# Kernel tuning notes

Measured on AMD Instinct MI355X. Metric: run time of the kernel, lower is better.

The kernel has to match this reference:

```python
import jax, jax.numpy as jnp
import numpy as np

MARGIN = 0.1
LAMBDA_EFFECT = 0.5

B, T_V, K, T_S = 32, 8192, 64, 128


def setup_inputs() -> dict:
    key = jax.random.key(0)
    k1, k2, k3, k4, k5 = jax.random.split(key, 5)
    pred_orig = jax.random.normal(k1, (B, T_V), dtype=jnp.float32)
    pred_intervened = jax.random.normal(k2, (K, B, T_V), dtype=jnp.float32)
    intervened_indices = jax.random.randint(k3, (K,), 0, T_S, dtype=jnp.int32)
    # GT alignment mask: sparse-ish binary alignment between frames and sentences
    gt_mask = jax.random.bernoulli(k4, 0.2, (B, T_V, T_S)).astype(jnp.int32)
    # prefix-valid video mask: valid length per batch in [T_V//2, T_V]
    lengths = jax.random.randint(k5, (B,), T_V // 2, T_V + 1, dtype=jnp.int32)
    mask_video = (jnp.arange(T_V, dtype=jnp.int32)[None, :] < lengths[:, None]).astype(jnp.int32)
    return {
        "pred_orig": pred_orig,
        "pred_intervened": pred_intervened,
        "intervened_indices": intervened_indices,
        "gt_mask": gt_mask,
        "mask_video": mask_video,
    }


def reference(pred_orig, pred_intervened, intervened_indices, gt_mask, mask_video):
    # pred_orig: [B,T], pred_intervened: [K,B,T], gt_mask: [B,T,S], mask_video: [B,T]
    prob_orig = jax.nn.sigmoid(pred_orig)                 # [B,T]
    prob_int = jax.nn.sigmoid(pred_intervened)            # [K,B,T]
    effect = jnp.abs(prob_orig[None, :, :] - prob_int)    # [K,B,T]

    valid = mask_video.astype(bool)                       # [B,T] (prefix mask == :T_v_valid slice)
    # gather intervened sentence columns: [B,T,K] -> [K,B,T]
    gt_sel = jnp.transpose(gt_mask[:, :, intervened_indices], (2, 0, 1))

    aligned = (gt_sel > 0) & valid[None]                  # [K,B,T]
    non_aligned = (gt_sel == 0) & valid[None]             # [K,B,T]

    cnt_a = aligned.sum(axis=-1)                          # [K,B]
    cnt_n = non_aligned.sum(axis=-1)                      # [K,B]

    ea = jnp.sum(effect * aligned, axis=-1) / jnp.maximum(cnt_a, 1)
    en = jnp.sum(effect * non_aligned, axis=-1) / jnp.maximum(cnt_n, 1)

    per_pair = jnp.where((cnt_a > 0) & (cnt_n > 0),
                         jax.nn.relu(MARGIN - (ea - en)),
                         jnp.zeros_like(ea))
    num_interventions = pred_orig.shape[0] * pred_intervened.shape[0]
    alignment_consistency = per_pair.sum() / max(num_interventions, 1)
    total_intervention_loss = alignment_consistency * LAMBDA_EFFECT
    return alignment_consistency, total_intervention_loss
```

## Files before the change

kernel.cpp:

```cpp
#include <hip/hip_runtime.h>
#include <cstdint>

#define BB 32
#define TV 8192
#define KK 64
#define TS 128
#define MARGIN_F 0.1f
#define LAMBDA_F 0.5f

typedef unsigned long long u64;
typedef unsigned int u32;

static constexpr int KB_PAIRS = KK * BB;
static constexpr int W32_PER_B = TV / 32;
static constexpr int W64_PER_B = TV / 64;
static constexpr int ROWS = 128;


__global__ __launch_bounds__(256, 2) void plane_kernel(
    const int* __restrict__ idx, const int* __restrict__ gt,
    const int* __restrict__ mv, u32* __restrict__ vbit, u32* __restrict__ pl,
    int* __restrict__ len, int* __restrict__ mw) {
  const int tid = threadIdx.x;
  const int lane = tid & 63;
  const int w = tid >> 6;
  const int blk = blockIdx.x;
  const int b = blk >> 6;
  const int tile = blk & 63;
  const int t0 = tile * ROWS;

  __shared__ u32 sV[4];
  __shared__ int gtile[ROWS * TS];

  const int rbase = b * TV + t0 + 32 * w;
  const int mvv = (lane < 32) ? mv[rbase + lane] : 0;
  const u32 V32 = (u32)__ballot(mvv != 0);
  const int g2 = t0 / 32 + w;
  if (lane == 0) {
    sV[w] = V32;
    vbit[b * W32_PER_B + g2] = V32;
    if (V32) {
      atomicAdd(&len[b], __popc(V32));
      atomicMax(&mw[b], g2);
    }
  }
  __syncthreads();

  u32* plbase = pl + (size_t)b * KK * W32_PER_B + g2;

  if ((sV[0] | sV[1] | sV[2] | sV[3]) == 0u) {
    plbase[(size_t)lane * W32_PER_B] = 0u;
    return;
  }

  {
    const char* gsrc = (const char*)(gt + (size_t)(b * TV + t0) * TS);
    char* lbase = (char*)gtile;
#pragma unroll
    for (int i = 0; i < 16; ++i) {
      const int off = (w * 16 + i) * 1024;
      __builtin_amdgcn_global_load_lds(
          (const __attribute__((address_space(1))) u32*)(gsrc + off +
                                                         lane * 16),
          (__attribute__((address_space(3))) u32*)(lbase + off), 16, 0, 0);
    }
  }
  __syncthreads();

  const int c = idx[lane];
  const int* col = gtile + 32 * w * TS + c;
  u32 plane = 0;
#pragma unroll
  for (int r = 0; r < 32; ++r)
    if (col[r * TS] > 0) plane |= 1u << r;
  plane &= sV[w];

  plbase[(size_t)lane * W32_PER_B] = plane;
}

__global__ __launch_bounds__(256, 4) void reduce_kernel(
    const float* __restrict__ po, const float* __restrict__ pi,
    const u32* __restrict__ vbit, const u32* __restrict__ pl,
    const int* __restrict__ mw,
    float* __restrict__ gsa, float* __restrict__ gsv,
    float* __restrict__ gca) {
  const int tid = threadIdx.x;
  const int lane = tid & 63;
  const int w = tid >> 6;
  const int kb = blockIdx.x;
  const int b = kb & (BB - 1);
  const int k = kb >> 5;
  const u64* plrow = (const u64*)pl + (size_t)(b * KK + k) * W64_PER_B;
  const u64* vrow = (const u64*)vbit + (size_t)b * W64_PER_B;
  const float* pirow = pi + (size_t)kb * TV;
  const float* porow = po + (size_t)b * TV;

  __shared__ float rs[4][2];
  __shared__ int rca;
  if (tid == 0) rca = 0;
  __syncthreads();

  const int nch = min(8, (mw[b] + 32) >> 5);
  const int sh = (tid & 15) * 4;
  float sa = 0.f, sv = 0.f;
#pragma unroll 2
  for (int c = 0; c < nch; ++c) {
    const int t = c * 1024 + tid * 4;
    const int widx = t >> 6;
    const u64 vw = vrow[widx];
    const u32 vb4 = (u32)((vw >> sh) & 15ull);
    if (vb4) {
      const u64 aw = plrow[widx];
      const u32 ab4 = (u32)((aw >> sh) & 15ull);
      const float4 x = *(const float4*)(pirow + t);
      const float4 p = *(const float4*)(porow + t);
      const float e0 =
          fabsf(__fdividef(1.f, 1.f + __expf(-p.x)) -
                __fdividef(1.f, 1.f + __expf(-x.x)));
      const float e1 =
          fabsf(__fdividef(1.f, 1.f + __expf(-p.y)) -
                __fdividef(1.f, 1.f + __expf(-x.y)));
      const float e2 =
          fabsf(__fdividef(1.f, 1.f + __expf(-p.z)) -
                __fdividef(1.f, 1.f + __expf(-x.z)));
      const float e3 =
          fabsf(__fdividef(1.f, 1.f + __expf(-p.w)) -
                __fdividef(1.f, 1.f + __expf(-x.w)));
      if (vb4 & 1u) sv += e0;
      if (vb4 & 2u) sv += e1;
      if (vb4 & 4u) sv += e2;
      if (vb4 & 8u) sv += e3;
      if (ab4 & 1u) sa += e0;
      if (ab4 & 2u) sa += e1;
      if (ab4 & 4u) sa += e2;
      if (ab4 & 8u) sa += e3;
    }
  }
#pragma unroll
  for (int off = 32; off; off >>= 1) {
    sa += __shfl_xor(sa, off);
    sv += __shfl_xor(sv, off);
  }
  if (lane == 0) {
    rs[w][0] = sa;
    rs[w][1] = sv;
  }
  if (tid < W64_PER_B) atomicAdd(&rca, __popcll(plrow[tid]));
  __syncthreads();
  if (tid == 0) {
    gsa[kb] = rs[0][0] + rs[1][0] + rs[2][0] + rs[3][0];
    gsv[kb] = rs[0][1] + rs[1][1] + rs[2][1] + rs[3][1];
    gca[kb] = (float)rca;
  }
}

__global__ __launch_bounds__(256) void fin_kernel(
    const float* __restrict__ gsa, const float* __restrict__ gsv,
    const float* __restrict__ gca, const int* __restrict__ len,
    float* __restrict__ out) {
  float s = 0.f;
  for (int i = threadIdx.x; i < KB_PAIRS; i += 256) {
    const int b = i & (BB - 1);
    const float ca = gca[i];
    const float cn = (float)len[b] - ca;
    if (ca > 0.f && cn > 0.f) {
      const float sa = gsa[i];
      const float sv = gsv[i];
      const float d = MARGIN_F - (sa / ca - (sv - sa) / cn);
      s += d > 0.f ? d : 0.f;
    }
  }
#pragma unroll
  for (int off = 32; off > 0; off >>= 1) s += __shfl_down(s, off);
  __shared__ float ws4[4];
  if ((threadIdx.x & 63) == 0) ws4[threadIdx.x >> 6] = s;
  __syncthreads();
  if (threadIdx.x == 0) {
    const float S = ws4[0] + ws4[1] + ws4[2] + ws4[3];
    const float ac = S * (1.0f / (float)KB_PAIRS);
    out[0] = ac;
    out[1] = ac * LAMBDA_F;
  }
}

extern "C" void kernel_launch(void* const* d_in, const int* in_sizes, int n_in,
                              void* d_out, int out_size, void* d_ws, size_t ws_size,
                              hipStream_t stream) {
  const float* pred_orig = (const float*)d_in[0];
  const float* pred_int  = (const float*)d_in[1];
  const int*   idx       = (const int*)d_in[2];
  const int*   gt        = (const int*)d_in[3];
  const int*   mv        = (const int*)d_in[4];
  float* out = (float*)d_out;

  float* gsa = (float*)d_ws;
  float* gsv = gsa + KB_PAIRS;
  float* gca = gsv + KB_PAIRS;
  int*   len = (int*)(gca + KB_PAIRS);
  int*   mw  = len + BB;
  u32*   vbit = (u32*)(mw + BB);
  u32*   pl   = vbit + BB * W32_PER_B;

  hipMemsetAsync(len, 0, 2 * BB * sizeof(int), stream);
  plane_kernel<<<BB * (TV / ROWS), 256, 0, stream>>>(idx, gt, mv, vbit, pl,
                                                     len, mw);
  reduce_kernel<<<KB_PAIRS, 256, 0, stream>>>(pred_orig, pred_int, vbit, pl,
                                              mw, gsa, gsv, gca);
  fin_kernel<<<1, 256, 0, stream>>>(gsa, gsv, gca, len, out);
}
```

Baseline: 285.8 us.

## Gather selected gt columns directly from global instead of staging tiles in LDS

The plane kernel no longer copies full 128-row gt tiles into shared memory. Each wave now reads only the gathered columns for its 32-row group straight from global memory into registers. Groups with no valid frames are skipped per wave rather than per block. This drops the LDS allocation and block barriers, raising occupancy, but it relies on scattered per-lane loads whose coalescing depends on the index pattern.

```diff
diff --git a/kernel.cpp b/kernel.cpp
--- a/kernel.cpp
+++ b/kernel.cpp
@@ -14,68 +14,43 @@
 static constexpr int KB_PAIRS = KK * BB;
 static constexpr int W32_PER_B = TV / 32;
 static constexpr int W64_PER_B = TV / 64;
-static constexpr int ROWS = 128;
 
 
-__global__ __launch_bounds__(256, 2) void plane_kernel(
+__global__ __launch_bounds__(256) void plane_kernel(
     const int* __restrict__ idx, const int* __restrict__ gt,
     const int* __restrict__ mv, u32* __restrict__ vbit, u32* __restrict__ pl,
     int* __restrict__ len, int* __restrict__ mw) {
-  const int tid = threadIdx.x;
-  const int lane = tid & 63;
-  const int w = tid >> 6;
+  const int lane = threadIdx.x & 63;
+  const int w = threadIdx.x >> 6;
   const int blk = blockIdx.x;
   const int b = blk >> 6;
   const int tile = blk & 63;
-  const int t0 = tile * ROWS;
+  const int g2 = tile * 4 + w;
+  const int grow = b * TV + g2 * 32;
 
-  __shared__ u32 sV[4];
-  __shared__ int gtile[ROWS * TS];
-
-  const int rbase = b * TV + t0 + 32 * w;
-  const int mvv = (lane < 32) ? mv[rbase + lane] : 0;
+  const int mvv = (lane < 32) ? mv[grow + lane] : 0;
   const u32 V32 = (u32)__ballot(mvv != 0);
-  const int g2 = t0 / 32 + w;
   if (lane == 0) {
-    sV[w] = V32;
     vbit[b * W32_PER_B + g2] = V32;
     if (V32) {
       atomicAdd(&len[b], __popc(V32));
       atomicMax(&mw[b], g2);
     }
   }
-  __syncthreads();
 
-  u32* plbase = pl + (size_t)b * KK * W32_PER_B + g2;
-
-  if ((sV[0] | sV[1] | sV[2] | sV[3]) == 0u) {
-    plbase[(size_t)lane * W32_PER_B] = 0u;
-    return;
+  u32 plane = 0;
+  if (V32) {
+    const int c = idx[lane];
+    const int* col = gt + (size_t)grow * TS + c;
+    int v[32];
+#pragma unroll
+    for (int r = 0; r < 32; ++r) v[r] = col[r * TS];
+#pragma unroll
+    for (int r = 0; r < 32; ++r)
+      if (v[r] > 0) plane |= 1u << r;
+    plane &= V32;
   }
-
-  {
-    const char* gsrc = (const char*)(gt + (size_t)(b * TV + t0) * TS);
-    char* lbase = (char*)gtile;
-#pragma unroll
-    for (int i = 0; i < 16; ++i) {
-      const int off = (w * 16 + i) * 1024;
-      __builtin_amdgcn_global_load_lds(
-          (const __attribute__((address_space(1))) u32*)(gsrc + off +
-                                                         lane * 16),
-          (__attribute__((address_space(3))) u32*)(lbase + off), 16, 0, 0);
-    }
-  }
-  __syncthreads();
-
-  const int c = idx[lane];
-  const int* col = gtile + 32 * w * TS + c;
-  u32 plane = 0;
-#pragma unroll
-  for (int r = 0; r < 32; ++r)
-    if (col[r * TS] > 0) plane |= 1u << r;
-  plane &= sV[w];
-
-  plbase[(size_t)lane * W32_PER_B] = plane;
+  pl[(size_t)(b * KK + lane) * W32_PER_B + g2] = plane;
 }
 
 __global__ __launch_bounds__(256, 4) void reduce_kernel(
@@ -202,8 +177,7 @@
   u32*   pl   = vbit + BB * W32_PER_B;
 
   hipMemsetAsync(len, 0, 2 * BB * sizeof(int), stream);
-  plane_kernel<<<BB * (TV / ROWS), 256, 0, stream>>>(idx, gt, mv, vbit, pl,
-                                                     len, mw);
+  plane_kernel<<<BB * 64, 256, 0, stream>>>(idx, gt, mv, vbit, pl, len, mw);
   reduce_kernel<<<KB_PAIRS, 256, 0, stream>>>(pred_orig, pred_int, vbit, pl,
                                               mw, gsa, gsv, gca);
   fin_kernel<<<1, 256, 0, stream>>>(gsa, gsv, gca, len, out);
```

Result: slower. 306.6 us (+7.3%).
